# Optimization experiments

Hardware: AMD Instinct MI355X
Metric: run time of the kernel (lower is better)

The kernel has to match this reference:

```python
import jax, jax.numpy as jnp
import numpy as np

D_MODEL = 1024
NUM_HEAD = 16


def setup_inputs() -> dict:
    key = jax.random.key(0)
    ks = jax.random.split(key, 11)
    B, S, D = 2, 2048, D_MODEL
    scale = 1.0 / np.sqrt(D)
    inp = {
        "Q": jax.random.normal(ks[0], (B, S, D), jnp.float32),
        "K": jax.random.normal(ks[1], (B, S, D), jnp.float32),
        "V": jax.random.normal(ks[2], (B, S, D), jnp.float32),
        "Wq": jax.random.normal(ks[3], (D, D), jnp.float32) * scale,
        "bq": jax.random.normal(ks[4], (D,), jnp.float32) * 0.01,
        "Wk": jax.random.normal(ks[5], (D, D), jnp.float32) * scale,
        "bk": jax.random.normal(ks[6], (D,), jnp.float32) * 0.01,
        "Wv": jax.random.normal(ks[7], (D, D), jnp.float32) * scale,
        "bv": jax.random.normal(ks[8], (D,), jnp.float32) * 0.01,
        "Wo": jax.random.normal(ks[9], (D, D), jnp.float32) * scale,
        "bo": jax.random.normal(ks[10], (D,), jnp.float32) * 0.01,
    }
    return inp


def reference(Q, K, V, Wq, bq, Wk, bk, Wv, bv, Wo, bo):
    b, vc, d_model = Q.shape
    h = NUM_HEAD
    hd = d_model // h
    # projections (torch Linear: x @ W.T + b)
    q = (Q @ Wq.T + bq).reshape(b, vc, h, hd)
    k = (K @ Wk.T + bk).reshape(b, vc, h, hd)
    v = (V @ Wv.T + bv).reshape(b, vc, h, hd)
    # scores [b,h,q,k]
    atten = jnp.einsum('bqhd,bkhd->bhqk', q, k) / np.sqrt(hd).astype(jnp.float32)
    atten = jax.nn.softmax(atten, axis=3)
    # weighted values -> [b,q,h,hd]
    out = jnp.einsum('bhqd,bdhv->bqhv', atten, v).reshape(b, vc, d_model)
    return out @ Wo.T + bo
```

## Files before the change

### kernel.cpp

```cpp
#include <hip/hip_runtime.h>

#define S_LEN 2048
#define DM 1024
#define NH 16
#define HD 64
#define NB 2

typedef unsigned short u16;
typedef __attribute__((ext_vector_type(8))) short s16x8;
typedef __attribute__((ext_vector_type(8))) unsigned short u16x8;
typedef __attribute__((ext_vector_type(4))) float fx4;
typedef __attribute__((ext_vector_type(2))) unsigned u32x2;
typedef __attribute__((ext_vector_type(4))) unsigned u32x4;

__device__ __forceinline__ u16 f2bf(float f) {
  unsigned u = __builtin_bit_cast(unsigned, f);
  return (u16)((u + 0x7FFFu + ((u >> 16) & 1u)) >> 16);
}

__device__ __forceinline__ unsigned cvt_pk_bf16(float a, float b) {
  unsigned r;
  asm("v_cvt_pk_bf16_f32 %0, %1, %2" : "=v"(r) : "v"(a), "v"(b));
  return r;
}

__device__ __forceinline__ void gload16(const void* g, void* l) {
  __builtin_amdgcn_global_load_lds(
      (const __attribute__((address_space(1))) unsigned*)g,
      (__attribute__((address_space(3))) unsigned*)l, 16, 0, 0);
}

__device__ __forceinline__ fx4 mfma16(s16x8 a, s16x8 b, fx4 c) {
  return __builtin_amdgcn_mfma_f32_16x16x32_bf16(a, b, c, 0, 0, 0);
}

__global__ __launch_bounds__(256) void cvt_all_kernel(
    const float* __restrict__ Q, const float* __restrict__ K,
    const float* __restrict__ V, const float* __restrict__ Wq,
    const float* __restrict__ Wk, const float* __restrict__ Wv,
    const float* __restrict__ Wo, u16* __restrict__ Qc, u16* __restrict__ Kc,
    u16* __restrict__ Vc, u16* __restrict__ Wqb, u16* __restrict__ Wkb,
    u16* __restrict__ Wvb, u16* __restrict__ Wob) {
  const int blk = blockIdx.x;
  const float* src;
  u16* dst;
  float scale = 1.0f;
  int off;
  if (blk < 2048)      { src = Q;  dst = Qc;  off = blk; }
  else if (blk < 4096) { src = K;  dst = Kc;  off = blk - 2048; }
  else if (blk < 6144) { src = V;  dst = Vc;  off = blk - 4096; }
  else if (blk < 6656) { src = Wq; dst = Wqb; off = blk - 6144; scale = 0.18033688f; }
  else if (blk < 7168) { src = Wk; dst = Wkb; off = blk - 6656; }
  else if (blk < 7680) { src = Wv; dst = Wvb; off = blk - 7168; }
  else                 { src = Wo; dst = Wob; off = blk - 7680; }
  const int i = (off * 256 + (int)threadIdx.x) * 8;
  fx4 a = *(const fx4*)(src + i);
  fx4 b = *(const fx4*)(src + i + 4);
  u16x8 o;
  o[0] = f2bf(a[0] * scale); o[1] = f2bf(a[1] * scale);
  o[2] = f2bf(a[2] * scale); o[3] = f2bf(a[3] * scale);
  o[4] = f2bf(b[0] * scale); o[5] = f2bf(b[1] * scale);
  o[6] = f2bf(b[2] * scale); o[7] = f2bf(b[3] * scale);
  *(u16x8*)(dst + i) = o;
}

__device__ __forceinline__ void store_out(u16* C, size_t idx, float v) { C[idx] = f2bf(v); }
__device__ __forceinline__ void store_out(float* C, size_t idx, float v) { C[idx] = v; }

template <typename OUT>
__device__ __forceinline__ void gemm_pipe_body(const u16* __restrict__ A,
                                               const u16* __restrict__ Bt,
                                               const float* __restrict__ bias,
                                               float bscale, OUT* __restrict__ C,
                                               u16* __restrict__ vt, bool vout,
                                               int m0, int n0) {
  __shared__ u16 Al[3][128 * 32];
  __shared__ u16 Bl[3][128 * 32];
  const int tid = threadIdx.x;
  const int wid = tid >> 6, lane = tid & 63;
  const int g = lane >> 4, lr = lane & 15;
  const int wr = wid >> 1, wc = wid & 1;
  const int row0 = tid >> 2, ch = tid & 3;
  const int chx = ch ^ ((row0 >> 1) & 3);

  fx4 acc[4][4] = {};

  auto stage = [&](u16* Ab, u16* Bb, int k0) {
    gload16(A + (size_t)(m0 + row0) * 1024 + k0 + chx * 8, (char*)Ab + wid * 1024);
    gload16(A + (size_t)(m0 + 64 + row0) * 1024 + k0 + chx * 8,
            (char*)Ab + 4096 + wid * 1024);
    gload16(Bt + (size_t)(n0 + row0) * 1024 + k0 + chx * 8, (char*)Bb + wid * 1024);
    gload16(Bt + (size_t)(n0 + 64 + row0) * 1024 + k0 + chx * 8,
            (char*)Bb + 4096 + wid * 1024);
  };
  auto readfrag = [&](const u16* Ab, const u16* Bb, s16x8* a, s16x8* b) {
#pragma unroll
    for (int m = 0; m < 4; ++m) {
      const int row = wr * 64 + m * 16 + lr;
      a[m] = *(const s16x8*)((const char*)Ab + row * 64 + (g ^ ((row >> 1) & 3)) * 16);
    }
#pragma unroll
    for (int n = 0; n < 4; ++n) {
      const int row = wc * 64 + n * 16 + lr;
      b[n] = *(const s16x8*)((const char*)Bb + row * 64 + (g ^ ((row >> 1) & 3)) * 16);
    }
  };
  auto domfma = [&](s16x8* a, s16x8* b) {
    __builtin_amdgcn_s_setprio(1);
#pragma unroll
    for (int m = 0; m < 4; ++m)
#pragma unroll
      for (int n = 0; n < 4; ++n) acc[m][n] = mfma16(a[m], b[n], acc[m][n]);
    __builtin_amdgcn_s_setprio(0);
  };

#define GSTEP(BUF, T, NW)                                                     \
  do {                                                                        \
    asm volatile("s_waitcnt vmcnt(" #NW ")" ::: "memory");                    \
    __builtin_amdgcn_s_barrier();                                             \
    __builtin_amdgcn_sched_barrier(0);                                        \
    s16x8 afr[4], bfr[4];                                                     \
    readfrag(Al[BUF], Bl[BUF], afr, bfr);                                     \
    asm volatile("s_waitcnt lgkmcnt(0)" ::: "memory");                        \
    __builtin_amdgcn_sched_barrier(0);                                        \
    __builtin_amdgcn_s_barrier();                                             \
    __builtin_amdgcn_sched_barrier(0);                                        \
    if ((T) + 3 < 32) stage(Al[BUF], Bl[BUF], ((T) + 3) * 32);                \
    domfma(afr, bfr);                                                         \
  } while (0)

  stage(Al[0], Bl[0], 0);
  stage(Al[1], Bl[1], 32);
  stage(Al[2], Bl[2], 64);

#pragma unroll 1
  for (int t = 0; t < 30; t += 3) {
    GSTEP(0, t, 8);
    GSTEP(1, t + 1, 8);
    GSTEP(2, t + 2, 8);
  }
  GSTEP(0, 30, 4);
  GSTEP(1, 31, 0);
#undef GSTEP

  if (vout) {
#pragma unroll
    for (int n = 0; n < 4; ++n) {
      const int col = n0 + wc * 64 + n * 16 + lr;
      const float bv = bias[col] * bscale;
      const int h = col >> 6, d = col & 63;
#pragma unroll
      for (int m = 0; m < 4; ++m) {
        const int row = m0 + wr * 64 + m * 16 + g * 4;
        const int bb = row >> 11, s = row & 2047;
        u32x2 w;
        w[0] = cvt_pk_bf16(acc[m][n][0] + bv, acc[m][n][1] + bv);
        w[1] = cvt_pk_bf16(acc[m][n][2] + bv, acc[m][n][3] + bv);
        *(u32x2*)(vt + ((size_t)(((bb << 4) | h) * 64 + d)) * 2048 + s) = w;
      }
    }
  } else {
#pragma unroll
    for (int n = 0; n < 4; ++n) {
      const int col = n0 + wc * 64 + n * 16 + lr;
      const float bv = bias[col] * bscale;
#pragma unroll
      for (int m = 0; m < 4; ++m) {
        const int row = m0 + wr * 64 + m * 16 + g * 4;
#pragma unroll
        for (int j = 0; j < 4; ++j)
          store_out(C, (size_t)(row + j) * 1024 + col, acc[m][n][j] + bv);
      }
    }
  }
}

__global__ __launch_bounds__(256, 3) void gemm_qkv_kernel(
    const u16* Qc, const u16* Kc, const u16* Vc, const u16* Wq, const u16* Wk,
    const u16* Wv, const float* bq, const float* bk, const float* bv, u16* q,
    u16* k, u16* vt) {
  const int hw = blockIdx.x + (blockIdx.y << 3) + (blockIdx.z << 8);
  const int xcd = hw & 7, j = hw >> 3;
  const int x = j & 7;
  const int p = xcd + ((j >> 3) << 3);
  const int y = p & 31, z = p >> 5;

  const u16 *Ap, *Bp;
  const float* bp;
  u16* Cp;
  float bs = 1.0f;
  bool vo = false;
  if (z == 0)      { Ap = Qc; Bp = Wq; bp = bq; Cp = q; bs = 0.18033688f; }
  else if (z == 1) { Ap = Kc; Bp = Wk; bp = bk; Cp = k; }
  else             { Ap = Vc; Bp = Wv; bp = bv; Cp = q; vo = true; }
  gemm_pipe_body<u16>(Ap, Bp, bp, bs, Cp, vt, vo, y * 128, x * 128);
}

__global__ __launch_bounds__(256, 3) void gemm_out_kernel(const u16* ctx,
                                                          const u16* Wo,
                                                          const float* bo,
                                                          float* out) {
  const int hw = blockIdx.x + (blockIdx.y << 3);
  const int xcd = hw & 7, j = hw >> 3;
  const int x = j & 7;
  const int y = xcd + ((j >> 3) << 3);
  gemm_pipe_body<float>(ctx, Wo, bo, 1.0f, out, nullptr, false, y * 128, x * 128);
}

__global__ __launch_bounds__(256, 4) void attn_kernel(const u16* __restrict__ qb,
                                                      const u16* __restrict__ kb,
                                                      const u16* __restrict__ vt,
                                                      u16* __restrict__ ctx) {
  __shared__ u16 Kl[2][64 * 64];
  __shared__ u16 Vl[2][64 * 64];
  __shared__ u16 Pl[4][16 * 64];

  const int tid = threadIdx.x, wid = tid >> 6, lane = tid & 63;
  const int g = lane >> 4, lr = lane & 15;
  const int rswz = (lr & 7) * 8;
  const int pswz = (lr & 7) * 16;
  char* Pb = (char*)&Pl[wid][0];

  const int hw = blockIdx.x;
  const int xcd = hw & 7, slot = hw >> 3;
  const int bh = xcd * 4 + (slot >> 5);
  const int b = bh >> 4, h = bh & 15;
  const int q0 = (slot & 31) * 64;

  const u16* qp = qb + ((size_t)(b * S_LEN + q0 + wid * 16 + lr)) * DM + h * HD;
  s16x8 aq[2];
  aq[0] = *(const s16x8*)(qp + g * 8);
  aq[1] = *(const s16x8*)(qp + 32 + g * 8);

  fx4 accO[4] = {};
  float lrun = 0.f;

  const int srow = tid >> 3, sch = tid & 7;
  const int schx = sch ^ (srow & 7);
  const u16* kbase = kb + ((size_t)b * S_LEN) * DM + h * HD;
  const u16* vtbase = vt + ((size_t)bh * 64) * S_LEN;

#define STAGE(buf, kv)                                                             \
  do {                                                                             \
    gload16(kbase + (size_t)((kv) + srow) * DM + schx * 8,                         \
            (char*)Kl[buf] + wid * 1024);                                          \
    gload16(kbase + (size_t)((kv) + 32 + srow) * DM + schx * 8,                    \
            (char*)Kl[buf] + 4096 + wid * 1024);                                   \
    gload16(vtbase + (size_t)srow * S_LEN + (kv) + schx * 8,                       \
            (char*)Vl[buf] + wid * 1024);                                          \
    gload16(vtbase + (size_t)(32 + srow) * S_LEN + (kv) + schx * 8,                \
            (char*)Vl[buf] + 4096 + wid * 1024);                                   \
  } while (0)

#define ASTEP(BUF, T, NW)                                                          \
  do {                                                                             \
    asm volatile("s_waitcnt vmcnt(" #NW ")" ::: "memory");                         \
    __builtin_amdgcn_s_barrier();                                                  \
    __builtin_amdgcn_sched_barrier(0);                                             \
    fx4 s[4] = {};                                                                 \
    s16x8 vf0[4], vf1[4];                                                          \
    __builtin_amdgcn_s_setprio(1);                                                 \
    _Pragma("unroll") for (int ks = 0; ks < 2; ++ks) {                             \
      _Pragma("unroll") for (int c = 0; c < 4; ++c) {                              \
        s16x8 kf = *(const s16x8*)(Kl[BUF] + (c * 16 + lr) * 64 +                  \
                                   ((ks * 32 + g * 8) ^ rswz));                    \
        s[c] = mfma16(kf, aq[ks], s[c]);                                           \
      }                                                                            \
    }                                                                              \
    __builtin_amdgcn_s_setprio(0);                                                 \
    _Pragma("unroll") for (int c = 0; c < 4; ++c) {                                \
      vf0[c] = *(const s16x8*)(Vl[BUF] + (c * 16 + lr) * 64 + ((g * 8) ^ rswz));   \
      vf1[c] =                                                                     \
          *(const s16x8*)(Vl[BUF] + (c * 16 + lr) * 64 + ((32 + g * 8) ^ rswz));   \
    }                                                                              \
    asm volatile("s_waitcnt lgkmcnt(0)" ::: "memory");                             \
    __builtin_amdgcn_sched_barrier(0);                                             \
    __builtin_amdgcn_s_barrier();                                                  \
    __builtin_amdgcn_sched_barrier(0);                                             \
    if ((T) + 2 < 32) STAGE(BUF, ((T) + 2) * 64);                                  \
     \
    _Pragma("unroll") for (int c = 0; c < 4; ++c)                                  \
        _Pragma("unroll") for (int j = 0; j < 4; ++j) s[c][j] =                    \
        __builtin_amdgcn_exp2f(s[c][j]);                                           \
    {                                                                              \
      const float r0 = (s[0][0] + s[0][1]) + (s[0][2] + s[0][3]);                  \
      const float r1 = (s[1][0] + s[1][1]) + (s[1][2] + s[1][3]);                  \
      const float r2 = (s[2][0] + s[2][1]) + (s[2][2] + s[2][3]);                  \
      const float r3 = (s[3][0] + s[3][1]) + (s[3][2] + s[3][3]);                  \
      lrun += (r0 + r1) + (r2 + r3);                                               \
    }                                                                              \
                     \
    _Pragma("unroll") for (int c = 0; c < 4; ++c) {                                \
      u32x2 w;                                                                     \
      w[0] = cvt_pk_bf16(s[c][0], s[c][1]);                                        \
      w[1] = cvt_pk_bf16(s[c][2], s[c][3]);                                        \
      *(u32x2*)(Pb + lr * 128 + ((c * 32 + g * 8) ^ pswz)) = w;                    \
    }                                                                              \
           \
    __builtin_amdgcn_s_setprio(1);                                                 \
    {                                                                              \
      s16x8 pb0 = *(const s16x8*)(Pb + lr * 128 + ((g * 16) ^ pswz));              \
      s16x8 pb1 = *(const s16x8*)(Pb + lr * 128 + ((64 + g * 16) ^ pswz));         \
      _Pragma("unroll") for (int c = 0; c < 4; ++c) {                              \
        accO[c] = mfma16(vf0[c], pb0, accO[c]);                                    \
        accO[c] = mfma16(vf1[c], pb1, accO[c]);                                    \
      }                                                                            \
    }                                                                              \
    __builtin_amdgcn_s_setprio(0);                                                 \
  } while (0)

  STAGE(0, 0);
  STAGE(1, 64);

#pragma unroll 1
  for (int t = 0; t < 30; t += 2) {
    ASTEP(0, t, 4);
    ASTEP(1, t + 1, 4);
  }
  ASTEP(0, 30, 4);
  ASTEP(1, 31, 0);
#undef ASTEP
#undef STAGE

  lrun += __shfl_xor(lrun, 16);
  lrun += __shfl_xor(lrun, 32);
  const float inv = 1.0f / lrun;
  u16* op = ctx + ((size_t)(b * S_LEN + q0 + wid * 16 + lr)) * DM + h * HD;
#pragma unroll
  for (int c = 0; c < 4; ++c) {
    u32x2 w;
    w[0] = cvt_pk_bf16(accO[c][0] * inv, accO[c][1] * inv);
    w[1] = cvt_pk_bf16(accO[c][2] * inv, accO[c][3] * inv);
    *(u32x2*)(op + c * 16 + g * 4) = w;
  }
}

extern "C" void kernel_launch(void* const* d_in, const int* in_sizes, int n_in,
                              void* d_out, int out_size, void* d_ws, size_t ws_size,
                              hipStream_t stream) {
  const float* Q = (const float*)d_in[0];
  const float* K = (const float*)d_in[1];
  const float* V = (const float*)d_in[2];
  const float* Wq = (const float*)d_in[3];
  const float* bq = (const float*)d_in[4];
  const float* Wk = (const float*)d_in[5];
  const float* bk = (const float*)d_in[6];
  const float* Wv = (const float*)d_in[7];
  const float* bv = (const float*)d_in[8];
  const float* Wo = (const float*)d_in[9];
  const float* bo = (const float*)d_in[10];
  float* out = (float*)d_out;

  char* ws = (char*)d_ws;
  const size_t SZ_T = (size_t)NB * S_LEN * DM * 2;
  const size_t SZ_W = (size_t)DM * DM * 2;

  u16* Wqb = (u16*)(ws);
  u16* Wkb = (u16*)(ws + SZ_W);
  u16* Wvb = (u16*)(ws + 2 * SZ_W);
  u16* Wob = (u16*)(ws + 3 * SZ_W);
  u16* Qc  = (u16*)(ws + 4 * SZ_W);
  u16* Kc  = (u16*)(ws + 4 * SZ_W + SZ_T);
  u16* Vc  = (u16*)(ws + 4 * SZ_W + 2 * SZ_T);
  u16* qb  = (u16*)(ws + 4 * SZ_W + 3 * SZ_T);
  u16* kb  = (u16*)(ws + 4 * SZ_W + 4 * SZ_T);
  u16* vtb = (u16*)(ws + 4 * SZ_W + 5 * SZ_T);
  u16* ctx = Qc;

  cvt_all_kernel<<<8192, 256, 0, stream>>>(Q, K, V, Wq, Wk, Wv, Wo, Qc, Kc, Vc,
                                           Wqb, Wkb, Wvb, Wob);

  gemm_qkv_kernel<<<dim3(8, 32, 3), 256, 0, stream>>>(Qc, Kc, Vc, Wqb, Wkb, Wvb,
                                                      bq, bk, bv, qb, kb, vtb);

  attn_kernel<<<1024, 256, 0, stream>>>(qb, kb, vtb, ctx);

  gemm_out_kernel<<<dim3(8, 32), 256, 0, stream>>>(ctx, Wob, bo, out);
}
```

Before: 119.0 us.

## Process 32 query rows per wave in attention to reuse K/V tiles

Each wave in the attention kernel now handles two 16-row query tiles, so every block covers 128 queries and the grid shrinks from 1024 to 512 blocks. Each K and V fragment read from LDS and each staged K/V tile feeds twice as many MFMAs, which halves global and LDS traffic per unit of work. In exchange, register use roughly doubles (launch bounds drop to 2 blocks per CU), and the smaller grid of 512 blocks may underfill the GPU's CUs, reducing latency hiding.

```diff
diff --git a/kernel.cpp b/kernel.cpp
--- a/kernel.cpp
+++ b/kernel.cpp
@@ -207,13 +207,13 @@
   gemm_pipe_body<float>(ctx, Wo, bo, 1.0f, out, nullptr, false, y * 128, x * 128);
 }
 
-__global__ __launch_bounds__(256, 4) void attn_kernel(const u16* __restrict__ qb,
+__global__ __launch_bounds__(256, 2) void attn_kernel(const u16* __restrict__ qb,
                                                       const u16* __restrict__ kb,
                                                       const u16* __restrict__ vt,
                                                       u16* __restrict__ ctx) {
   __shared__ u16 Kl[2][64 * 64];
   __shared__ u16 Vl[2][64 * 64];
-  __shared__ u16 Pl[4][16 * 64];
+  __shared__ u16 Pl[4][32 * 64];
 
   const int tid = threadIdx.x, wid = tid >> 6, lane = tid & 63;
   const int g = lane >> 4, lr = lane & 15;
@@ -223,17 +223,19 @@
 
   const int hw = blockIdx.x;
   const int xcd = hw & 7, slot = hw >> 3;
-  const int bh = xcd * 4 + (slot >> 5);
+  const int bh = xcd * 4 + (slot >> 4);
   const int b = bh >> 4, h = bh & 15;
-  const int q0 = (slot & 31) * 64;
-
-  const u16* qp = qb + ((size_t)(b * S_LEN + q0 + wid * 16 + lr)) * DM + h * HD;
-  s16x8 aq[2];
-  aq[0] = *(const s16x8*)(qp + g * 8);
-  aq[1] = *(const s16x8*)(qp + 32 + g * 8);
-
-  fx4 accO[4] = {};
-  float lrun = 0.f;
+  const int q0 = (slot & 15) * 128;
+
+  const u16* qp = qb + ((size_t)(b * S_LEN + q0 + wid * 32 + lr)) * DM + h * HD;
+  s16x8 aq0[2], aq1[2];
+  aq0[0] = *(const s16x8*)(qp + g * 8);
+  aq0[1] = *(const s16x8*)(qp + 32 + g * 8);
+  aq1[0] = *(const s16x8*)(qp + (size_t)16 * DM + g * 8);
+  aq1[1] = *(const s16x8*)(qp + (size_t)16 * DM + 32 + g * 8);
+
+  fx4 accO0[4] = {}, accO1[4] = {};
+  float lrun0 = 0.f, lrun1 = 0.f;
 
   const int srow = tid >> 3, sch = tid & 7;
   const int schx = sch ^ (srow & 7);
@@ -257,14 +259,15 @@
     asm volatile("s_waitcnt vmcnt(" #NW ")" ::: "memory");                         \
     __builtin_amdgcn_s_barrier();                                                  \
     __builtin_amdgcn_sched_barrier(0);                                             \
-    fx4 s[4] = {};                                                                 \
+    fx4 s0[4] = {}, s1[4] = {};                                                    \
     s16x8 vf0[4], vf1[4];                                                          \
     __builtin_amdgcn_s_setprio(1);                                                 \
     _Pragma("unroll") for (int ks = 0; ks < 2; ++ks) {                             \
       _Pragma("unroll") for (int c = 0; c < 4; ++c) {                              \
         s16x8 kf = *(const s16x8*)(Kl[BUF] + (c * 16 + lr) * 64 +                  \
                                    ((ks * 32 + g * 8) ^ rswz));                    \
-        s[c] = mfma16(kf, aq[ks], s[c]);                                           \
+        s0[c] = mfma16(kf, ks ? aq0[1] : aq0[0], s0[c]);                           \
+        s1[c] = mfma16(kf, ks ? aq1[1] : aq1[0], s1[c]);                           \
       }                                                                            \
     }                                                                              \
     __builtin_amdgcn_s_setprio(0);                                                 \
@@ -278,32 +281,43 @@
     __builtin_amdgcn_s_barrier();                                                  \
     __builtin_amdgcn_sched_barrier(0);                                             \
     if ((T) + 2 < 32) STAGE(BUF, ((T) + 2) * 64);                                  \
-     \
+      \
     _Pragma("unroll") for (int c = 0; c < 4; ++c)                                  \
-        _Pragma("unroll") for (int j = 0; j < 4; ++j) s[c][j] =                    \
-        __builtin_amdgcn_exp2f(s[c][j]);                                           \
-    {                                                                              \
-      const float r0 = (s[0][0] + s[0][1]) + (s[0][2] + s[0][3]);                  \
-      const float r1 = (s[1][0] + s[1][1]) + (s[1][2] + s[1][3]);                  \
-      const float r2 = (s[2][0] + s[2][1]) + (s[2][2] + s[2][3]);                  \
-      const float r3 = (s[3][0] + s[3][1]) + (s[3][2] + s[3][3]);                  \
-      lrun += (r0 + r1) + (r2 + r3);                                               \
+        _Pragma("unroll") for (int j = 0; j < 4; ++j) {                            \
+      s0[c][j] = __builtin_amdgcn_exp2f(s0[c][j]);                                 \
+      s1[c][j] = __builtin_amdgcn_exp2f(s1[c][j]);                                 \
     }                                                                              \
+    lrun0 += ((s0[0][0] + s0[0][1]) + (s0[0][2] + s0[0][3])) +                     \
+             ((s0[1][0] + s0[1][1]) + (s0[1][2] + s0[1][3])) +                     \
+             ((s0[2][0] + s0[2][1]) + (s0[2][2] + s0[2][3])) +                     \
+             ((s0[3][0] + s0[3][1]) + (s0[3][2] + s0[3][3]));                      \
+    lrun1 += ((s1[0][0] + s1[0][1]) + (s1[0][2] + s1[0][3])) +                     \
+             ((s1[1][0] + s1[1][1]) + (s1[1][2] + s1[1][3])) +                     \
+             ((s1[2][0] + s1[2][1]) + (s1[2][2] + s1[2][3])) +                     \
+             ((s1[3][0] + s1[3][1]) + (s1[3][2] + s1[3][3]));                      \
                      \
     _Pragma("unroll") for (int c = 0; c < 4; ++c) {                                \
-      u32x2 w;                                                                     \
-      w[0] = cvt_pk_bf16(s[c][0], s[c][1]);                                        \
-      w[1] = cvt_pk_bf16(s[c][2], s[c][3]);                                        \
-      *(u32x2*)(Pb + lr * 128 + ((c * 32 + g * 8) ^ pswz)) = w;                    \
+      u32x2 w0, w1;                                                                \
+      w0[0] = cvt_pk_bf16(s0[c][0], s0[c][1]);                                     \
+      w0[1] = cvt_pk_bf16(s0[c][2], s0[c][3]);                                     \
+      w1[0] = cvt_pk_bf16(s1[c][0], s1[c][1]);                                     \
+      w1[1] = cvt_pk_bf16(s1[c][2], s1[c][3]);                                     \
+      *(u32x2*)(Pb + lr * 128 + ((c * 32 + g * 8) ^ pswz)) = w0;                   \
+      *(u32x2*)(Pb + (16 + lr) * 128 + ((c * 32 + g * 8) ^ pswz)) = w1;            \
     }                                                                              \
-           \
+                                         \
     __builtin_amdgcn_s_setprio(1);                                                 \
     {                                                                              \
-      s16x8 pb0 = *(const s16x8*)(Pb + lr * 128 + ((g * 16) ^ pswz));              \
-      s16x8 pb1 = *(const s16x8*)(Pb + lr * 128 + ((64 + g * 16) ^ pswz));         \
+      s16x8 pb00 = *(const s16x8*)(Pb + lr * 128 + ((g * 16) ^ pswz));             \
+      s16x8 pb01 = *(const s16x8*)(Pb + lr * 128 + ((64 + g * 16) ^ pswz));        \
+      s16x8 pb10 = *(const s16x8*)(Pb + (16 + lr) * 128 + ((g * 16) ^ pswz));      \
+      s16x8 pb11 =                                                                 \
+          *(const s16x8*)(Pb + (16 + lr) * 128 + ((64 + g * 16) ^ pswz));          \
       _Pragma("unroll") for (int c = 0; c < 4; ++c) {                              \
-        accO[c] = mfma16(vf0[c], pb0, accO[c]);                                    \
-        accO[c] = mfma16(vf1[c], pb1, accO[c]);                                    \
+        accO0[c] = mfma16(vf0[c], pb00, accO0[c]);                                 \
+        accO0[c] = mfma16(vf1[c], pb01, accO0[c]);                                 \
+        accO1[c] = mfma16(vf0[c], pb10, accO1[c]);                                 \
+        accO1[c] = mfma16(vf1[c], pb11, accO1[c]);                                 \
       }                                                                            \
     }                                                                              \
     __builtin_amdgcn_s_setprio(0);                                                 \
@@ -322,16 +336,23 @@
 #undef ASTEP
 #undef STAGE
 
-  lrun += __shfl_xor(lrun, 16);
-  lrun += __shfl_xor(lrun, 32);
-  const float inv = 1.0f / lrun;
-  u16* op = ctx + ((size_t)(b * S_LEN + q0 + wid * 16 + lr)) * DM + h * HD;
+  lrun0 += __shfl_xor(lrun0, 16);
+  lrun0 += __shfl_xor(lrun0, 32);
+  lrun1 += __shfl_xor(lrun1, 16);
+  lrun1 += __shfl_xor(lrun1, 32);
+  const float inv0 = 1.0f / lrun0;
+  const float inv1 = 1.0f / lrun1;
+  u16* op0 = ctx + ((size_t)(b * S_LEN + q0 + wid * 32 + lr)) * DM + h * HD;
+  u16* op1 = op0 + (size_t)16 * DM;
 #pragma unroll
   for (int c = 0; c < 4; ++c) {
-    u32x2 w;
-    w[0] = cvt_pk_bf16(accO[c][0] * inv, accO[c][1] * inv);
-    w[1] = cvt_pk_bf16(accO[c][2] * inv, accO[c][3] * inv);
-    *(u32x2*)(op + c * 16 + g * 4) = w;
+    u32x2 w0, w1;
+    w0[0] = cvt_pk_bf16(accO0[c][0] * inv0, accO0[c][1] * inv0);
+    w0[1] = cvt_pk_bf16(accO0[c][2] * inv0, accO0[c][3] * inv0);
+    w1[0] = cvt_pk_bf16(accO1[c][0] * inv1, accO1[c][1] * inv1);
+    w1[1] = cvt_pk_bf16(accO1[c][2] * inv1, accO1[c][3] * inv1);
+    *(u32x2*)(op0 + c * 16 + g * 4) = w0;
+    *(u32x2*)(op1 + c * 16 + g * 4) = w1;
   }
 }
 
@@ -373,7 +394,7 @@
   gemm_qkv_kernel<<<dim3(8, 32, 3), 256, 0, stream>>>(Qc, Kc, Vc, Wqb, Wkb, Wvb,
                                                       bq, bk, bv, qb, kb, vtb);
 
-  attn_kernel<<<1024, 256, 0, stream>>>(qb, kb, vtb, ctx);
+  attn_kernel<<<512, 256, 0, stream>>>(qb, kb, vtb, ctx);
 
   gemm_out_kernel<<<dim3(8, 32), 256, 0, stream>>>(ctx, Wob, bo, out);
 }
```

Result: faster. 111.0 us, median of 2 (-6.8%).
